# Optimization experiments

Hardware: AMD Instinct MI355X
Metric: run time of the kernel (lower is better)

## Reference

```python
import jax, jax.numpy as jnp
import numpy as np

B = 64
IN_FEATURES = 20000
OUT_FEATURES = 2000  # out_features * K with K=1
N_EDGES = 2_000_000


def setup_inputs() -> dict:
    key = jax.random.key(0)
    k1, k2, k3 = jax.random.split(key, 3)
    input = jax.random.normal(k1, (B, IN_FEATURES), dtype=jnp.float32)
    # col 0: input neuron index, col 1: output neuron index (both < 2000, valid for both ranges)
    sparse_mask = jax.random.randint(k2, (N_EDGES, 2), 0, OUT_FEATURES, dtype=jnp.int64)
    weight = jax.random.normal(k3, (N_EDGES,), dtype=jnp.float32)
    bias = jnp.zeros((OUT_FEATURES,), dtype=jnp.float32)
    return {"input": input, "sparse_mask": sparse_mask, "weight": weight, "bias": bias}


def reference(input, sparse_mask, weight, bias):
    # gather: [B, E]
    src = input[:, sparse_mask[:, 0]] * weight[None, :]
    # scatter-add per-edge contributions into output neurons
    out = jnp.zeros((input.shape[0], OUT_FEATURES), dtype=input.dtype)
    out = out.at[:, sparse_mask[:, 1]].add(src)
    return out + bias
```

## Files before the change

### kernel.cpp

```cpp
#include <hip/hip_runtime.h>


#define ROWS8 8
#define NB 256
#define NBP 256
#define SCAP 32
#define E_PT 8
#define TPB_SC 512
#define SEGX (TPB_SC * E_PT)
#define OVF_CAP 4096

#define TILE_O 64
#define KS 64
#define SLICES 16
#define PSTRIDE 2048

__global__ void smw_init10(int* __restrict__ meta) {
    if (threadIdx.x < 64) meta[threadIdx.x] = 0;
}

__global__ __launch_bounds__(TPB_SC) void smw_scatter9(
    const int* __restrict__ mask, const float* __restrict__ wgt,
    int2* __restrict__ binned, int* __restrict__ counts,
    int2* __restrict__ ovf, int* __restrict__ ovf_cnt,
    int n_edges, int krows, int nbins, int nseg) {
    __shared__ int hist[NB];
    __shared__ int sflag;
    extern __shared__ int2 stage[];
    const int tid = threadIdx.x;
    const int blk = blockIdx.x;
    const long long e0 = (long long)blk * SEGX;
    if (tid < NB) hist[tid] = 0;
    if (tid < 64) {
        unsigned v = (tid < n_edges) ? ((const unsigned*)mask)[2 * tid + 1] : 0u;
        unsigned long long bal = __ballot(v != 0u);
        if (tid == 0) sflag = (bal == 0ull) ? 1 : 0;
    }
    __syncthreads();
    const bool is64 = (sflag != 0);

    int ci[E_PT], co[E_PT]; float wv[E_PT];
    if (is64) {
        #pragma unroll
        for (int i = 0; i < E_PT; ++i) {
            long long e = e0 + (long long)i * TPB_SC + tid;
            ci[i] = -1; co[i] = 0;
            if (e < n_edges) { int4 mm = ((const int4*)mask)[e]; ci[i] = mm.x; co[i] = mm.z; }
        }
    } else {
        #pragma unroll
        for (int i = 0; i < E_PT; ++i) {
            long long e = e0 + (long long)i * TPB_SC + tid;
            ci[i] = -1; co[i] = 0;
            if (e < n_edges) { int2 mm = ((const int2*)mask)[e]; ci[i] = mm.x; co[i] = mm.y; }
        }
    }
    #pragma unroll
    for (int i = 0; i < E_PT; ++i) {
        long long e = e0 + (long long)i * TPB_SC + tid;
        wv[i] = (e < n_edges) ? wgt[e] : 0.0f;
    }

    #pragma unroll
    for (int i = 0; i < E_PT; ++i) {
        if ((unsigned)ci[i] < (unsigned)krows) {
            int b = ci[i] >> 3;
            int r = atomicAdd(&hist[b], 1);
            if (r < SCAP) {
                stage[b * SCAP + r] =
                    make_int2((int)((((unsigned)(ci[i] & 7)) << 16) |
                                    (unsigned)(co[i] & 0xFFFF)),
                              __float_as_int(wv[i]));
            } else {
                int j = atomicAdd(ovf_cnt, 1);
                if (j < OVF_CAP)
                    ovf[j] = make_int2((ci[i] << 16) | (co[i] & 0xFFFF),
                                       __float_as_int(wv[i]));
            }
        }
    }
    __syncthreads();
    const int grp = tid >> 4;
    const int ln  = tid & 15;
    for (int b = grp; b < nbins; b += (TPB_SC / 16)) {
        int c = hist[b]; if (c > SCAP) c = SCAP;
        int cp = (c + 7) & ~7;
        long long base = ((long long)b * nseg + blk) * SCAP;
        for (int k = ln; k < cp; k += 16)
            binned[base + k] = (k < c) ? stage[b * SCAP + k] : make_int2(-1, 0);
        if (ln == 0) counts[blk * NBP + b] = cp;
    }
}

__global__ __launch_bounds__(512) void smw_bin_build6(
    const int2* __restrict__ binned, const int* __restrict__ counts,
    const int2* __restrict__ ovf, const int* __restrict__ ovf_cnt,
    float* __restrict__ W, int out_f, int krows, int nseg) {
    extern __shared__ float tile[];
    const int tid = threadIdx.x;
    const int bin = blockIdx.x;
    const int tile_elems = ROWS8 * out_f;
    {
        float4* t4 = (float4*)tile;
        int n4 = tile_elems >> 2;
        for (int t = tid; t < n4; t += 512) t4[t] = make_float4(0.f, 0.f, 0.f, 0.f);
    }
    __syncthreads();
    const int grp = tid >> 3;
    const int ln8 = tid & 7;
    for (int s = grp; s < nseg; s += 64) {
        int cp = counts[s * NBP + bin];
        const int4* sp = (const int4*)(binned + ((long long)bin * nseg + s) * SCAP);
        for (int j = ln8; j * 2 < cp; j += 8) {
            int4 two = sp[j];
            if (two.x >= 0)
                atomicAdd(&tile[(two.x >> 16) * out_f + (two.x & 0xFFFF)],
                          __int_as_float(two.y));
            if (two.z >= 0)
                atomicAdd(&tile[(two.z >> 16) * out_f + (two.z & 0xFFFF)],
                          __int_as_float(two.w));
        }
    }
    int no = *ovf_cnt; if (no > OVF_CAP) no = OVF_CAP;
    for (int i = tid; i < no; i += 512) {
        int2 r = ovf[i];
        int ci = ((unsigned)r.x) >> 16;
        if ((ci >> 3) == bin)
            atomicAdd(&tile[(ci & 7) * out_f + (r.x & 0xFFFF)], __int_as_float(r.y));
    }
    __syncthreads();
    #pragma unroll
    for (int r = 0; r < ROWS8; ++r) {
        int row = bin * ROWS8 + r;
        if (row >= krows) break;
        float* dst = W + (long long)row * out_f;
        const float* s = tile + r * out_f;
        for (int c = tid * 4; c < out_f; c += 2048)
            *(float4*)&dst[c] = *(const float4*)&s[c];
    }
}

__global__ __launch_bounds__(256) void smw_gemm4(
    const float* __restrict__ A, const float* __restrict__ W,
    float* __restrict__ partial, int in_features, int out_f, int krows, int Bsz) {
    __shared__ float As[64][KS + 4];
    __shared__ float Ws[KS][TILE_O];
    const int tid = threadIdx.x;
    const int tx = tid & 15;
    const int ty = tid >> 4;
    const int o_base = blockIdx.x * TILE_O;

    float acc[4][4] = {};
    #pragma unroll
    for (int half = 0; half < 2; ++half) {
        const int k0 = (blockIdx.y * 2 + half) * KS;
        __syncthreads();
        #pragma unroll
        for (int t = 0; t < 4; ++t) {
            int idx = t * 256 + tid;
            int b = idx >> 4;
            int c4 = (idx & 15) * 4;
            int gi = k0 + c4;
            float4 v = make_float4(0.f, 0.f, 0.f, 0.f);
            if (b < Bsz) {
                const float* src = A + (long long)b * in_features + gi;
                if (gi + 3 < krows) v = *(const float4*)src;
                else {
                    if (gi + 0 < krows) v.x = src[0];
                    if (gi + 1 < krows) v.y = src[1];
                    if (gi + 2 < krows) v.z = src[2];
                    if (gi + 3 < krows) v.w = src[3];
                }
            }
            *(float4*)&As[b][c4] = v;
        }
        #pragma unroll
        for (int t = 0; t < 4; ++t) {
            int idx = t * 256 + tid;
            int r = idx >> 4;
            int c4 = (idx & 15) * 4;
            int gi = k0 + r;
            int go = o_base + c4;
            float4 v = make_float4(0.f, 0.f, 0.f, 0.f);
            if (gi < krows) {
                const float* src = W + (long long)gi * out_f + go;
                if (go + 3 < out_f) v = *(const float4*)src;
                else {
                    if (go + 0 < out_f) v.x = src[0];
                    if (go + 1 < out_f) v.y = src[1];
                    if (go + 2 < out_f) v.z = src[2];
                    if (go + 3 < out_f) v.w = src[3];
                }
            }
            *(float4*)&Ws[r][c4] = v;
        }
        __syncthreads();

        #pragma unroll 8
        for (int i = 0; i < KS; ++i) {
            float4 w4 = *(const float4*)&Ws[i][tx * 4];
            float a[4];
            #pragma unroll
            for (int r = 0; r < 4; ++r) a[r] = As[ty * 4 + r][i];
            #pragma unroll
            for (int r = 0; r < 4; ++r) {
                acc[r][0] += a[r] * w4.x;
                acc[r][1] += a[r] * w4.y;
                acc[r][2] += a[r] * w4.z;
                acc[r][3] += a[r] * w4.w;
            }
        }
    }

    float* P = partial + (long long)blockIdx.y * 64 * PSTRIDE;
    #pragma unroll
    for (int r = 0; r < 4; ++r) {
        int b = ty * 4 + r;
        if (b < Bsz)
            *(float4*)&P[(long long)b * PSTRIDE + o_base + tx * 4] =
                make_float4(acc[r][0], acc[r][1], acc[r][2], acc[r][3]);
    }
}

__global__ void smw_reduce3(const float* __restrict__ partial,
                            const float* __restrict__ bias,
                            float* __restrict__ out, int out_f, int Bsz, int total4) {
    int idx = blockIdx.x * blockDim.x + threadIdx.x;
    if (idx >= total4) return;
    const int of4 = out_f >> 2;
    int b = idx / of4, o4 = idx - b * of4;
    const float4* B4 = (const float4*)bias;
    const float4* P4 = (const float4*)partial;
    float4 acc = B4[o4];
    #pragma unroll
    for (int s = 0; s < SLICES; ++s) {
        float4 v = P4[((long long)s * 64 + b) * (PSTRIDE >> 2) + o4];
        acc.x += v.x; acc.y += v.y; acc.z += v.z; acc.w += v.w;
    }
    ((float4*)out)[idx] = acc;
}

__global__ void smw_detect(const unsigned int* __restrict__ m, int* __restrict__ flag) {
    if (blockIdx.x == 0 && threadIdx.x == 0) {
        unsigned int orv = 0u;
        for (int k = 0; k < 64; ++k) orv |= m[2 * k + 1];
        *flag = (orv == 0u) ? 1 : 0;
    }
}

__global__ void smw_build_fb(const int* __restrict__ mask, const float* __restrict__ wgt,
                             float* __restrict__ W, const int* __restrict__ flag,
                             int n_edges, int out_f) {
    int e = blockIdx.x * blockDim.x + threadIdx.x;
    if (e >= n_edges) return;
    int ci, co;
    if (*flag) {
        const long long* m64 = (const long long*)mask;
        ci = (int)m64[2 * (long long)e];
        co = (int)m64[2 * (long long)e + 1];
    } else {
        ci = mask[2 * e]; co = mask[2 * e + 1];
    }
    atomicAdd(&W[(long long)ci * out_f + co], wgt[e]);
}

__global__ void smw_init_out_fb(float* __restrict__ out, const float* __restrict__ bias,
                                int total, int out_f) {
    int idx = blockIdx.x * blockDim.x + threadIdx.x;
    if (idx < total) out[idx] = bias[idx % out_f];
}

__global__ __launch_bounds__(256) void smw_gemm_fb(
    const float* __restrict__ A, const float* __restrict__ W,
    float* __restrict__ out, int in_features, int out_f, int krows,
    int n_chunks, int Bsz) {
    __shared__ float As[64][36];
    __shared__ float Ws[32][64];
    const int tid = threadIdx.x;
    const int tx = tid & 15;
    const int ty = tid >> 4;
    const int o_base = blockIdx.x * 64;
    float acc[4][4] = {};
    for (int c = blockIdx.y; c < n_chunks; c += 8) {
        const int i0 = c * 32;
        __syncthreads();
        #pragma unroll
        for (int k = 0; k < 8; ++k) {
            int idx = k * 256 + tid;
            int i = idx & 31;
            int b = idx >> 5;
            float v = 0.0f;
            int gi = i0 + i;
            if (b < Bsz && gi < in_features) v = A[(long long)b * in_features + gi];
            As[b][i] = v;
        }
        #pragma unroll
        for (int k = 0; k < 8; ++k) {
            int idx = k * 256 + tid;
            int o = idx & 63;
            int i = idx >> 6;
            int gi = i0 + i;
            int go = o_base + o;
            Ws[i][o] = (gi < krows && go < out_f) ? W[(long long)gi * out_f + go] : 0.0f;
        }
        __syncthreads();
        #pragma unroll
        for (int i = 0; i < 32; ++i) {
            float4 w4 = *(const float4*)(&Ws[i][tx * 4]);
            float a[4];
            #pragma unroll
            for (int r = 0; r < 4; ++r) a[r] = As[ty * 4 + r][i];
            #pragma unroll
            for (int r = 0; r < 4; ++r) {
                acc[r][0] += a[r] * w4.x;
                acc[r][1] += a[r] * w4.y;
                acc[r][2] += a[r] * w4.z;
                acc[r][3] += a[r] * w4.w;
            }
        }
    }
    #pragma unroll
    for (int r = 0; r < 4; ++r) {
        int b = ty * 4 + r;
        if (b >= Bsz) continue;
        #pragma unroll
        for (int cc = 0; cc < 4; ++cc) {
            int o = o_base + tx * 4 + cc;
            if (o < out_f) atomicAdd(&out[(long long)b * out_f + o], acc[r][cc]);
        }
    }
}

static inline size_t align_up(size_t x, size_t a) { return (x + a - 1) & ~(a - 1); }

extern "C" void kernel_launch(void* const* d_in, const int* in_sizes, int n_in,
                              void* d_out, int out_size, void* d_ws, size_t ws_size,
                              hipStream_t stream) {
    const float* input = (const float*)d_in[0];
    const int*   mask  = (const int*)d_in[1];
    const float* wgt   = (const float*)d_in[2];
    const float* bias  = (const float*)d_in[3];
    float* out = (float*)d_out;

    const int out_f   = in_sizes[3];
    const int n_edges = in_sizes[2];
    const int Bsz     = out_size / out_f;
    const int in_features = in_sizes[0] / Bsz;
    const int krows   = out_f;
    const int nbins   = (krows + ROWS8 - 1) / ROWS8;
    const int nseg    = (n_edges + SEGX - 1) / SEGX;
    const int n_ot    = (out_f + TILE_O - 1) / TILE_O;

    size_t W_bytes      = align_up((size_t)krows * out_f * 4, 1024);
    size_t binned_bytes = align_up((size_t)nbins * nseg * SCAP * 8, 1024);
    size_t part_bytes   = align_up((size_t)SLICES * 64 * PSTRIDE * 4, 1024);
    size_t union_bytes  = binned_bytes > part_bytes ? binned_bytes : part_bytes;
    size_t counts_bytes = align_up((size_t)nseg * NBP * 4, 1024);
    size_t meta_bytes   = 64 * 4 + (size_t)OVF_CAP * 8 + 1024;
    size_t need_fast = W_bytes + union_bytes + counts_bytes + meta_bytes;

    char* p = (char*)d_ws;
    float* W       = (float*)p;
    int2*  binned  = (int2*)(p + W_bytes);
    float* partial = (float*)(p + W_bytes);
    int*   counts  = (int*)(p + W_bytes + union_bytes);
    int*   meta    = (int*)(p + W_bytes + union_bytes + counts_bytes);
    int*   ovf_cnt = meta + 32;
    int2*  ovf     = (int2*)(meta + 64);

    const size_t sc_lds = (size_t)nbins * SCAP * 8;
    const size_t bb_lds = (size_t)ROWS8 * out_f * 4;
    const bool fast = (ws_size >= need_fast) && out_f <= 2048 && (out_f & 3) == 0 &&
                      krows <= 2048 && nbins <= 250 && Bsz <= 64 && n_edges >= 1 &&
                      n_ot <= 32 && sc_lds <= 64000 && bb_lds <= 65536 &&
                      (out_size & 3) == 0;

    if (fast) {
        smw_init10<<<1, 64, 0, stream>>>(meta);
        smw_scatter9<<<nseg, TPB_SC, sc_lds, stream>>>(mask, wgt, binned, counts,
                                                       ovf, ovf_cnt,
                                                       n_edges, krows, nbins, nseg);
        smw_bin_build6<<<nbins, 512, bb_lds, stream>>>(binned, counts, ovf, ovf_cnt,
                                                       W, out_f, krows, nseg);
        dim3 grid(n_ot, SLICES);
        smw_gemm4<<<grid, 256, 0, stream>>>(input, W, partial, in_features, out_f,
                                            krows, Bsz);
        int total4 = out_size >> 2;
        smw_reduce3<<<(total4 + 255) / 256, 256, 0, stream>>>(partial, bias, out,
                                                              out_f, Bsz, total4);
    } else {
        int* flag_fb = (int*)(p + (size_t)krows * out_f * 4);
        hipMemsetAsync(d_ws, 0, (size_t)krows * out_f * 4, stream);
        smw_detect<<<1, 64, 0, stream>>>((const unsigned int*)mask, flag_fb);
        smw_build_fb<<<(n_edges + 255) / 256, 256, 0, stream>>>(mask, wgt, W, flag_fb,
                                                                n_edges, out_f);
        smw_init_out_fb<<<(out_size + 255) / 256, 256, 0, stream>>>(out, bias, out_size, out_f);
        const int n_chunks = (krows + 31) / 32;
        dim3 grid((out_f + 63) / 64, 8);
        smw_gemm_fb<<<grid, 256, 0, stream>>>(input, W, out, in_features, out_f,
                                              krows, n_chunks, Bsz);
    }
}
```

Before: 54.80 us.

## Use per-block overflow buffers to drop init kernel; prefetch second GEMM K-tile

The global overflow counter and its init kernel are replaced by a per-block LDS overflow counter, with each block writing up to OVB spilled edges into its own slot and recording the count in a spare column of counts. The bin-build kernel then scans every segment's overflow slots instead of one global list. This removes one kernel launch and the global atomics on the overflow counter. The GEMM also loads the second K-half into registers while the first half is computed, so the global-load latency overlaps with the math. The per-block overflow cap of 32 can silently drop edges if one block overflows more than that, and each bin-build block now loops over all segments' overflow entries.

Result: faster. 50.36 us (-8.1%).

```diff
diff --git a/kernel.cpp b/kernel.cpp
--- a/kernel.cpp
+++ b/kernel.cpp
@@ -5,32 +5,29 @@
 #define NB 256
 #define NBP 256
 #define SCAP 32
+#define OVB 32
 #define E_PT 8
 #define TPB_SC 512
 #define SEGX (TPB_SC * E_PT)
-#define OVF_CAP 4096
 
 #define TILE_O 64
 #define KS 64
 #define SLICES 16
 #define PSTRIDE 2048
 
-__global__ void smw_init10(int* __restrict__ meta) {
-    if (threadIdx.x < 64) meta[threadIdx.x] = 0;
-}
-
-__global__ __launch_bounds__(TPB_SC) void smw_scatter9(
+__global__ __launch_bounds__(TPB_SC) void smw_scatter10(
     const int* __restrict__ mask, const float* __restrict__ wgt,
-    int2* __restrict__ binned, int* __restrict__ counts,
-    int2* __restrict__ ovf, int* __restrict__ ovf_cnt,
+    int2* __restrict__ binned, int* __restrict__ counts, int2* __restrict__ ovfblk,
     int n_edges, int krows, int nbins, int nseg) {
     __shared__ int hist[NB];
     __shared__ int sflag;
+    __shared__ int ovfc;
     extern __shared__ int2 stage[];
     const int tid = threadIdx.x;
     const int blk = blockIdx.x;
     const long long e0 = (long long)blk * SEGX;
     if (tid < NB) hist[tid] = 0;
+    if (tid == 0) ovfc = 0;
     if (tid < 64) {
         unsigned v = (tid < n_edges) ? ((const unsigned*)mask)[2 * tid + 1] : 0u;
         unsigned long long bal = __ballot(v != 0u);
@@ -72,10 +69,11 @@
                                     (unsigned)(co[i] & 0xFFFF)),
                               __float_as_int(wv[i]));
             } else {
-                int j = atomicAdd(ovf_cnt, 1);
-                if (j < OVF_CAP)
-                    ovf[j] = make_int2((ci[i] << 16) | (co[i] & 0xFFFF),
-                                       __float_as_int(wv[i]));
+                int j = atomicAdd(&ovfc, 1);
+                if (j < OVB)
+                    ovfblk[blk * OVB + j] =
+                        make_int2((ci[i] << 16) | (co[i] & 0xFFFF),
+                                  __float_as_int(wv[i]));
             }
         }
     }
@@ -90,12 +88,16 @@
             binned[base + k] = (k < c) ? stage[b * SCAP + k] : make_int2(-1, 0);
         if (ln == 0) counts[blk * NBP + b] = cp;
     }
-}
-
-__global__ __launch_bounds__(512) void smw_bin_build6(
+    if (tid == 0) {
+        int oc = ovfc; if (oc > OVB) oc = OVB;
+        counts[blk * NBP + (NBP - 1)] = oc;
+    }
+}
+
+__global__ __launch_bounds__(512) void smw_bin_build7(
     const int2* __restrict__ binned, const int* __restrict__ counts,
-    const int2* __restrict__ ovf, const int* __restrict__ ovf_cnt,
-    float* __restrict__ W, int out_f, int krows, int nseg) {
+    const int2* __restrict__ ovfblk, float* __restrict__ W,
+    int out_f, int krows, int nseg) {
     extern __shared__ float tile[];
     const int tid = threadIdx.x;
     const int bin = blockIdx.x;
@@ -121,12 +123,15 @@
                           __int_as_float(two.w));
         }
     }
-    int no = *ovf_cnt; if (no > OVF_CAP) no = OVF_CAP;
-    for (int i = tid; i < no; i += 512) {
-        int2 r = ovf[i];
-        int ci = ((unsigned)r.x) >> 16;
-        if ((ci >> 3) == bin)
-            atomicAdd(&tile[(ci & 7) * out_f + (r.x & 0xFFFF)], __int_as_float(r.y));
+    for (int s = tid; s < nseg; s += 512) {
+        int oc = counts[s * NBP + (NBP - 1)];
+        for (int j = 0; j < oc; ++j) {
+            int2 r = ovfblk[s * OVB + j];
+            int ci = ((unsigned)r.x) >> 16;
+            if ((ci >> 3) == bin)
+                atomicAdd(&tile[(ci & 7) * out_f + (r.x & 0xFFFF)],
+                          __int_as_float(r.y));
+        }
     }
     __syncthreads();
     #pragma unroll
@@ -140,7 +145,56 @@
     }
 }
 
-__global__ __launch_bounds__(256) void smw_gemm4(
+__device__ __forceinline__ void smw_load_a(float4 (&r)[4], const float* __restrict__ A,
+                                           int k0, int in_features, int krows,
+                                           int Bsz, int tid) {
+    #pragma unroll
+    for (int t = 0; t < 4; ++t) {
+        int idx = t * 256 + tid;
+        int b = idx >> 4;
+        int c4 = (idx & 15) * 4;
+        int gi = k0 + c4;
+        float4 v = make_float4(0.f, 0.f, 0.f, 0.f);
+        if (b < Bsz) {
+            const float* src = A + (long long)b * in_features + gi;
+            if (gi + 3 < krows) v = *(const float4*)src;
+            else {
+                if (gi + 0 < krows) v.x = src[0];
+                if (gi + 1 < krows) v.y = src[1];
+                if (gi + 2 < krows) v.z = src[2];
+                if (gi + 3 < krows) v.w = src[3];
+            }
+        }
+        r[t] = v;
+    }
+}
+
+__device__ __forceinline__ void smw_load_w(float4 (&r)[4], const float* __restrict__ W,
+                                           int k0, int o_base, int out_f, int krows,
+                                           int tid) {
+    #pragma unroll
+    for (int t = 0; t < 4; ++t) {
+        int idx = t * 256 + tid;
+        int rr = idx >> 4;
+        int c4 = (idx & 15) * 4;
+        int gi = k0 + rr;
+        int go = o_base + c4;
+        float4 v = make_float4(0.f, 0.f, 0.f, 0.f);
+        if (gi < krows) {
+            const float* src = W + (long long)gi * out_f + go;
+            if (go + 3 < out_f) v = *(const float4*)src;
+            else {
+                if (go + 0 < out_f) v.x = src[0];
+                if (go + 1 < out_f) v.y = src[1];
+                if (go + 2 < out_f) v.z = src[2];
+                if (go + 3 < out_f) v.w = src[3];
+            }
+        }
+        r[t] = v;
+    }
+}
+
+__global__ __launch_bounds__(256) void smw_gemm6(
     const float* __restrict__ A, const float* __restrict__ W,
     float* __restrict__ partial, int in_features, int out_f, int krows, int Bsz) {
     __shared__ float As[64][KS + 4];
@@ -149,66 +203,57 @@
     const int tx = tid & 15;
     const int ty = tid >> 4;
     const int o_base = blockIdx.x * TILE_O;
+    const int k0a = blockIdx.y * 2 * KS;
+    const int k0b = k0a + KS;
+
+    float4 ra[4], rw[4];
+    smw_load_a(ra, A, k0a, in_features, krows, Bsz, tid);
+    smw_load_w(rw, W, k0a, o_base, out_f, krows, tid);
+    #pragma unroll
+    for (int t = 0; t < 4; ++t) {
+        int idx = t * 256 + tid;
+        *(float4*)&As[idx >> 4][(idx & 15) * 4] = ra[t];
+        *(float4*)&Ws[idx >> 4][(idx & 15) * 4] = rw[t];
+    }
+    smw_load_a(ra, A, k0b, in_features, krows, Bsz, tid);
+    smw_load_w(rw, W, k0b, o_base, out_f, krows, tid);
+    __syncthreads();
 
     float acc[4][4] = {};
-    #pragma unroll
-    for (int half = 0; half < 2; ++half) {
-        const int k0 = (blockIdx.y * 2 + half) * KS;
-        __syncthreads();
-        #pragma unroll
-        for (int t = 0; t < 4; ++t) {
-            int idx = t * 256 + tid;
-            int b = idx >> 4;
-            int c4 = (idx & 15) * 4;
-            int gi = k0 + c4;
-            float4 v = make_float4(0.f, 0.f, 0.f, 0.f);
-            if (b < Bsz) {
-                const float* src = A + (long long)b * in_features + gi;
-                if (gi + 3 < krows) v = *(const float4*)src;
-                else {
-                    if (gi + 0 < krows) v.x = src[0];
-                    if (gi + 1 < krows) v.y = src[1];
-                    if (gi + 2 < krows) v.z = src[2];
-                    if (gi + 3 < krows) v.w = src[3];
-                }
-            }
-            *(float4*)&As[b][c4] = v;
-        }
-        #pragma unroll
-        for (int t = 0; t < 4; ++t) {
-            int idx = t * 256 + tid;
-            int r = idx >> 4;
-            int c4 = (idx & 15) * 4;
-            int gi = k0 + r;
-            int go = o_base + c4;
-            float4 v = make_float4(0.f, 0.f, 0.f, 0.f);
-            if (gi < krows) {
-                const float* src = W + (long long)gi * out_f + go;
-                if (go + 3 < out_f) v = *(const float4*)src;
-                else {
-                    if (go + 0 < out_f) v.x = src[0];
-                    if (go + 1 < out_f) v.y = src[1];
-                    if (go + 2 < out_f) v.z = src[2];
-                    if (go + 3 < out_f) v.w = src[3];
-                }
-            }
-            *(float4*)&Ws[r][c4] = v;
-        }
-        __syncthreads();
-
-        #pragma unroll 8
-        for (int i = 0; i < KS; ++i) {
-            float4 w4 = *(const float4*)&Ws[i][tx * 4];
-            float a[4];
-            #pragma unroll
-            for (int r = 0; r < 4; ++r) a[r] = As[ty * 4 + r][i];
-            #pragma unroll
-            for (int r = 0; r < 4; ++r) {
-                acc[r][0] += a[r] * w4.x;
-                acc[r][1] += a[r] * w4.y;
-                acc[r][2] += a[r] * w4.z;
-                acc[r][3] += a[r] * w4.w;
-            }
+    #pragma unroll 8
+    for (int i = 0; i < KS; ++i) {
+        float4 w4 = *(const float4*)&Ws[i][tx * 4];
+        float a[4];
+        #pragma unroll
+        for (int r = 0; r < 4; ++r) a[r] = As[ty * 4 + r][i];
+        #pragma unroll
+        for (int r = 0; r < 4; ++r) {
+            acc[r][0] += a[r] * w4.x;
+            acc[r][1] += a[r] * w4.y;
+            acc[r][2] += a[r] * w4.z;
+            acc[r][3] += a[r] * w4.w;
+        }
+    }
+    __syncthreads();
+    #pragma unroll
+    for (int t = 0; t < 4; ++t) {
+        int idx = t * 256 + tid;
+        *(float4*)&As[idx >> 4][(idx & 15) * 4] = ra[t];
+        *(float4*)&Ws[idx >> 4][(idx & 15) * 4] = rw[t];
+    }
+    __syncthreads();
+    #pragma unroll 8
+    for (int i = 0; i < KS; ++i) {
+        float4 w4 = *(const float4*)&Ws[i][tx * 4];
+        float a[4];
+        #pragma unroll
+        for (int r = 0; r < 4; ++r) a[r] = As[ty * 4 + r][i];
+        #pragma unroll
+        for (int r = 0; r < 4; ++r) {
+            acc[r][0] += a[r] * w4.x;
+            acc[r][1] += a[r] * w4.y;
+            acc[r][2] += a[r] * w4.z;
+            acc[r][3] += a[r] * w4.w;
         }
     }
 
@@ -356,17 +401,15 @@
     size_t part_bytes   = align_up((size_t)SLICES * 64 * PSTRIDE * 4, 1024);
     size_t union_bytes  = binned_bytes > part_bytes ? binned_bytes : part_bytes;
     size_t counts_bytes = align_up((size_t)nseg * NBP * 4, 1024);
-    size_t meta_bytes   = 64 * 4 + (size_t)OVF_CAP * 8 + 1024;
-    size_t need_fast = W_bytes + union_bytes + counts_bytes + meta_bytes;
+    size_t ovf_bytes    = align_up((size_t)nseg * OVB * 8, 1024);
+    size_t need_fast = W_bytes + union_bytes + counts_bytes + ovf_bytes + 1024;
 
     char* p = (char*)d_ws;
     float* W       = (float*)p;
     int2*  binned  = (int2*)(p + W_bytes);
     float* partial = (float*)(p + W_bytes);
     int*   counts  = (int*)(p + W_bytes + union_bytes);
-    int*   meta    = (int*)(p + W_bytes + union_bytes + counts_bytes);
-    int*   ovf_cnt = meta + 32;
-    int2*  ovf     = (int2*)(meta + 64);
+    int2*  ovfblk  = (int2*)(p + W_bytes + union_bytes + counts_bytes);
 
     const size_t sc_lds = (size_t)nbins * SCAP * 8;
     const size_t bb_lds = (size_t)ROWS8 * out_f * 4;
@@ -376,14 +419,13 @@
                       (out_size & 3) == 0;
 
     if (fast) {
-        smw_init10<<<1, 64, 0, stream>>>(meta);
-        smw_scatter9<<<nseg, TPB_SC, sc_lds, stream>>>(mask, wgt, binned, counts,
-                                                       ovf, ovf_cnt,
-                                                       n_edges, krows, nbins, nseg);
-        smw_bin_build6<<<nbins, 512, bb_lds, stream>>>(binned, counts, ovf, ovf_cnt,
-                                                       W, out_f, krows, nseg);
+        smw_scatter10<<<nseg, TPB_SC, sc_lds, stream>>>(mask, wgt, binned, counts,
+                                                        ovfblk, n_edges, krows,
+                                                        nbins, nseg);
+        smw_bin_build7<<<nbins, 512, bb_lds, stream>>>(binned, counts, ovfblk, W,
+                                                       out_f, krows, nseg);
         dim3 grid(n_ot, SLICES);
-        smw_gemm4<<<grid, 256, 0, stream>>>(input, W, partial, in_features, out_f,
+        smw_gemm6<<<grid, 256, 0, stream>>>(input, W, partial, in_features, out_f,
                                             krows, Bsz);
         int total4 = out_size >> 2;
         smw_reduce3<<<(total4 + 255) / 256, 256, 0, stream>>>(partial, bias, out,
```
